# Performance work log

Measured on AMD Instinct MI355X. Metric: run time of the kernel, lower is better.

Reference implementation:

```python
import jax, jax.numpy as jnp
import numpy as np
from jax import lax


def setup_inputs() -> dict:
    key = jax.random.key(0)
    kx, kw = jax.random.split(key)
    X = jax.random.normal(kx, (16, 64, 224, 224), dtype=jnp.float32)
    W = jax.random.normal(kw, (1, 1, 3, 3), dtype=jnp.float32)
    return {"X": X, "W": W}


def reference(X, W):
    # Original: ZeroPad2d(1), then slide a single (k,k) filter over every
    # channel independently (filter broadcasts over B and C; sum over k,k).
    # This is a depthwise conv where every channel shares the SAME kernel.
    B, C, H, Wd = X.shape
    Xp = jnp.pad(X, ((0, 0), (0, 0), (1, 1), (1, 1)))  # ZeroPad2d(1)
    kern = jnp.tile(W, (C, 1, 1, 1))  # (C, 1, k, k) — shared weights per channel
    out = lax.conv_general_dilated(
        Xp, kern,
        window_strides=(1, 1),
        padding='VALID',
        dimension_numbers=('NCHW', 'OIHW', 'NCHW'),
        feature_group_count=C,
    )
    return out  # [B, C, 224, 224]
```

## Files before the change

### kernel.cpp

```cpp
#include <hip/hip_runtime.h>


#define HH 224
#define WW 224
#define X4T 56
#define Y4T 56

__global__ __launch_bounds__(256) void dwconv3x3_shared_w(
    const float* __restrict__ X, const float* __restrict__ Wk,
    float* __restrict__ Out, int nTiles)
{
    int idx = blockIdx.x * 256 + threadIdx.x;
    if (idx >= nTiles) return;

    int x4 = idx % X4T;
    int t  = idx / X4T;
    int y4 = t % Y4T;
    int p  = t / Y4T;

    const float w00 = Wk[0], w01 = Wk[1], w02 = Wk[2];
    const float w10 = Wk[3], w11 = Wk[4], w12 = Wk[5];
    const float w20 = Wk[6], w21 = Wk[7], w22 = Wk[8];

    const int x0 = x4 * 4;
    const int y0 = y4 * 4;
    const float* plane  = X   + (size_t)p * (HH * WW);
    float*       oplane = Out + (size_t)p * (HH * WW);

    float row[6][6];
    #pragma unroll
    for (int r = 0; r < 6; ++r) {
        const int yr = y0 - 1 + r;
        const bool yok = (yr >= 0) && (yr < HH);
        const float* rp = plane + yr * WW + x0;
        float4 v = yok ? *(const float4*)rp : make_float4(0.f, 0.f, 0.f, 0.f);
        row[r][0] = (yok && x0 > 0)      ? rp[-1] : 0.f;
        row[r][1] = v.x;
        row[r][2] = v.y;
        row[r][3] = v.z;
        row[r][4] = v.w;
        row[r][5] = (yok && x0 + 4 < WW) ? rp[4]  : 0.f;
    }

    #pragma unroll
    for (int j = 0; j < 4; ++j) {
        float4 o;
        float* op = (float*)&o;
        #pragma unroll
        for (int c = 0; c < 4; ++c) {
            float acc;
            acc  = w00 * row[j + 0][c + 0] + w01 * row[j + 0][c + 1] + w02 * row[j + 0][c + 2];
            acc += w10 * row[j + 1][c + 0] + w11 * row[j + 1][c + 1] + w12 * row[j + 1][c + 2];
            acc += w20 * row[j + 2][c + 0] + w21 * row[j + 2][c + 1] + w22 * row[j + 2][c + 2];
            op[c] = acc;
        }
        *(float4*)(oplane + (y0 + j) * WW + x0) = o;
    }
}

extern "C" void kernel_launch(void* const* d_in, const int* in_sizes, int n_in,
                              void* d_out, int out_size, void* d_ws, size_t ws_size,
                              hipStream_t stream) {
    const float* X  = (const float*)d_in[0];
    const float* Wk = (const float*)d_in[1];
    float* Out = (float*)d_out;

    const int nPlanes = 16 * 64;
    const int nTiles  = nPlanes * X4T * Y4T;
    const int threads = 256;
    const int blocks  = (nTiles + threads - 1) / threads;

    dwconv3x3_shared_w<<<blocks, threads, 0, stream>>>(X, Wk, Out, nTiles);
}
```

Measured before the change: 343.7 us.

## Process vertical 28-row strips per thread with rolling row registers

Each thread now walks down a 28-row strip of 4-wide columns and keeps a rolling three-row register window. This replaces independent 4x4 tiles that each reloaded six rows. The aim is to cut redundant halo loads, from 1.5x to about 1.07x row reads, and to lower index-math overhead. Output stores also become nontemporal to avoid polluting the cache. The trade-off is about 8x fewer threads (458k) and a serial dependency chain per thread, which lowers memory-level parallelism.

```diff
diff --git a/kernel.cpp b/kernel.cpp
--- a/kernel.cpp
+++ b/kernel.cpp
@@ -4,57 +4,69 @@
 #define HH 224
 #define WW 224
 #define X4T 56
-#define Y4T 56
+#define STRIPS 8
+#define SH 28
 
-__global__ __launch_bounds__(256) void dwconv3x3_shared_w(
+typedef float f4 __attribute__((ext_vector_type(4)));
+
+__device__ __forceinline__ void load_row6(float r[6], const float* rp,
+                                          bool yok, bool xl, bool xr) {
+    if (yok) {
+        f4 v = *(const f4*)rp;
+        r[0] = xl ? rp[-1] : 0.f;
+        r[1] = v.x; r[2] = v.y; r[3] = v.z; r[4] = v.w;
+        r[5] = xr ? rp[4] : 0.f;
+    } else {
+        r[0] = r[1] = r[2] = r[3] = r[4] = r[5] = 0.f;
+    }
+}
+
+__global__ __launch_bounds__(256) void dwconv3x3_strip(
     const float* __restrict__ X, const float* __restrict__ Wk,
-    float* __restrict__ Out, int nTiles)
+    float* __restrict__ Out, int nThreads)
 {
     int idx = blockIdx.x * 256 + threadIdx.x;
-    if (idx >= nTiles) return;
+    if (idx >= nThreads) return;
 
-    int x4 = idx % X4T;
-    int t  = idx / X4T;
-    int y4 = t % Y4T;
-    int p  = t / Y4T;
+    int x4    = idx % X4T;
+    int t     = idx / X4T;
+    int strip = t % STRIPS;
+    int p     = t / STRIPS;
 
     const float w00 = Wk[0], w01 = Wk[1], w02 = Wk[2];
     const float w10 = Wk[3], w11 = Wk[4], w12 = Wk[5];
     const float w20 = Wk[6], w21 = Wk[7], w22 = Wk[8];
 
-    const int x0 = x4 * 4;
-    const int y0 = y4 * 4;
-    const float* plane  = X   + (size_t)p * (HH * WW);
-    float*       oplane = Out + (size_t)p * (HH * WW);
+    const int  x0 = x4 * 4;
+    const int  y0 = strip * SH;
+    const bool xl = (x0 > 0);
+    const bool xr = (x0 + 4 < WW);
 
-    float row[6][6];
-    #pragma unroll
-    for (int r = 0; r < 6; ++r) {
-        const int yr = y0 - 1 + r;
-        const bool yok = (yr >= 0) && (yr < HH);
-        const float* rp = plane + yr * WW + x0;
-        float4 v = yok ? *(const float4*)rp : make_float4(0.f, 0.f, 0.f, 0.f);
-        row[r][0] = (yok && x0 > 0)      ? rp[-1] : 0.f;
-        row[r][1] = v.x;
-        row[r][2] = v.y;
-        row[r][3] = v.z;
-        row[r][4] = v.w;
-        row[r][5] = (yok && x0 + 4 < WW) ? rp[4]  : 0.f;
-    }
+    const float* plane  = X   + (size_t)p * (HH * WW) + x0;
+    float*       oplane = Out + (size_t)p * (HH * WW) + x0;
 
-    #pragma unroll
-    for (int j = 0; j < 4; ++j) {
-        float4 o;
-        float* op = (float*)&o;
+    float a[6], b[6], c[6];
+    load_row6(a, plane + (y0 - 1) * WW, y0 > 0, xl, xr);
+    load_row6(b, plane + (y0    ) * WW, true,   xl, xr);
+
+    #pragma unroll 4
+    for (int j = 0; j < SH; ++j) {
+        const int yn = y0 + j + 1;
+        load_row6(c, plane + yn * WW, yn < HH, xl, xr);
+
+        f4 o;
         #pragma unroll
-        for (int c = 0; c < 4; ++c) {
+        for (int ci = 0; ci < 4; ++ci) {
             float acc;
-            acc  = w00 * row[j + 0][c + 0] + w01 * row[j + 0][c + 1] + w02 * row[j + 0][c + 2];
-            acc += w10 * row[j + 1][c + 0] + w11 * row[j + 1][c + 1] + w12 * row[j + 1][c + 2];
-            acc += w20 * row[j + 2][c + 0] + w21 * row[j + 2][c + 1] + w22 * row[j + 2][c + 2];
-            op[c] = acc;
+            acc  = w00 * a[ci] + w01 * a[ci + 1] + w02 * a[ci + 2];
+            acc += w10 * b[ci] + w11 * b[ci + 1] + w12 * b[ci + 2];
+            acc += w20 * c[ci] + w21 * c[ci + 1] + w22 * c[ci + 2];
+            o[ci] = acc;
         }
-        *(float4*)(oplane + (y0 + j) * WW + x0) = o;
+        __builtin_nontemporal_store(o, (f4*)(oplane + (y0 + j) * WW));
+
+        #pragma unroll
+        for (int q = 0; q < 6; ++q) { a[q] = b[q]; b[q] = c[q]; }
     }
 }
 
@@ -65,10 +77,10 @@
     const float* Wk = (const float*)d_in[1];
     float* Out = (float*)d_out;
 
-    const int nPlanes = 16 * 64;
-    const int nTiles  = nPlanes * X4T * Y4T;
-    const int threads = 256;
-    const int blocks  = (nTiles + threads - 1) / threads;
+    const int nPlanes  = 16 * 64;
+    const int nThreads = nPlanes * STRIPS * X4T;
+    const int threads  = 256;
+    const int blocks   = (nThreads + threads - 1) / threads;
 
-    dwconv3x3_shared_w<<<blocks, threads, 0, stream>>>(X, Wk, Out, nTiles);
+    dwconv3x3_strip<<<blocks, threads, 0, stream>>>(X, Wk, Out, nThreads);
 }
```

Measured after the change: 356.8 us. 3.8% more time.
